# Optimization experiments

Measured on AMD Instinct MI355X. Metric: run time of the kernel, lower is better.

The kernel has to match this reference:

```python
import jax, jax.numpy as jnp
import numpy as np

act = jax.nn.softplus

def _lin(h, W, b):
    return h @ W + b

def _residual_stack(h, Ws, bs):
    # Ws: [L,2,D,D], bs: [L,2,D]; Residual: x + Lin(act(Lin(act(x))))
    for i in range(Ws.shape[0]):
        t = _lin(act(h), Ws[i, 0], bs[i, 0])
        t = _lin(act(t), Ws[i, 1], bs[i, 1])
        h = t + h
    return h

def setup_inputs() -> dict:
    key = jax.random.key(0)
    N, E, D, R = 40000, 640000, 128, 64
    n_int, n_atomic, n_out = 2, 2, 1
    ks = jax.random.split(key, 24)
    s = 1.0 / np.sqrt(D)
    sr = 1.0 / np.sqrt(R)
    inp = {
        'x': jax.random.normal(ks[0], (N, D), jnp.float32),
        'g_ij': jax.random.uniform(ks[1], (E, R), jnp.float32),
        'idx_i': jax.random.randint(ks[2], (E,), 0, N, jnp.int32),
        'idx_j': jax.random.randint(ks[3], (E,), 0, N, jnp.int32),
        'n_atoms': N,
        'u': jax.random.uniform(ks[4], (D,), jnp.float32),  # torch.rand(n_atom_basis)
        'W_g': jax.random.normal(ks[5], (R, D), jnp.float32) * sr,
        'b_g': jnp.zeros((D,), jnp.float32),
        'W_j': jax.random.normal(ks[6], (D, D), jnp.float32) * s,
        'b_j': jnp.zeros((D,), jnp.float32),
        'W_i': jax.random.normal(ks[7], (D, D), jnp.float32) * s,
        'b_i': jnp.zeros((D,), jnp.float32),
        'W_f': jax.random.normal(ks[8], (D, D), jnp.float32) * s,
        'b_f': jnp.zeros((D,), jnp.float32),
        'Wres_int': jax.random.normal(ks[9], (n_int, 2, D, D), jnp.float32) * s,
        'bres_int': jnp.zeros((n_int, 2, D), jnp.float32),
        'Wres_atom': jax.random.normal(ks[10], (n_atomic, 2, D, D), jnp.float32) * s,
        'bres_atom': jnp.zeros((n_atomic, 2, D), jnp.float32),
        'Wres_out': jax.random.normal(ks[11], (n_out, 2, D, D), jnp.float32) * s,
        'bres_out': jnp.zeros((n_out, 2, D), jnp.float32),
        'W_out': jax.random.normal(ks[12], (D, D), jnp.float32) * s,
        'b_out': jnp.zeros((D,), jnp.float32),
    }
    return inp

def reference(x, g_ij, idx_i, idx_j, n_atoms, u,
              W_g, b_g, W_j, b_j, W_i, b_i, W_f, b_f,
              Wres_int, bres_int, Wres_atom, bres_atom,
              Wres_out, bres_out, W_out, b_out):
    # --- PhysNetInteraction ---
    x_j = x[idx_j]                                   # [E,D] gather
    xp = u * x                                       # random feature scale
    vp = act(_lin(act(x_j), W_j, b_j)) * _lin(g_ij, W_g, b_g)   # [E,D]
    vm = act(_lin(act(x), W_i, b_i))                 # [N,D]
    v = jax.ops.segment_sum(vp, idx_i, num_segments=n_atoms) + vm
    v = _residual_stack(v, Wres_int, bres_int)
    v = act(v)
    h = xp + _lin(v, W_f, b_f)
    # --- atomic residuals ---
    h = _residual_stack(h, Wres_atom, bres_atom)
    # --- Output block ---
    o = _residual_stack(h, Wres_out, bres_out)
    o = _lin(act(o), W_out, b_out)
    return (o, h)
```

## Files before the change

### kernel.cpp

```cpp
#include <hip/hip_runtime.h>


#define D 128
#define TILE 64
#define LDP 136
#define SLOT 16384
#define EPB 64

typedef __attribute__((ext_vector_type(8))) short s8v;
typedef __attribute__((ext_vector_type(4))) unsigned short us4;
typedef __attribute__((ext_vector_type(4))) float f32x4;

struct Frag { f32x4 v[8]; };
struct WReg8 { s8v w[8]; };

__device__ __forceinline__ float sp_act(float x) {
    float t = __builtin_amdgcn_exp2f(-fabsf(x) * 1.44269504088896f);
    return fmaxf(x, 0.f) + 0.69314718055994f * __builtin_amdgcn_logf(1.0f + t);
}
__device__ __forceinline__ unsigned short f2bf(float f) {
    unsigned int u = __float_as_uint(f);
    u += 0x7fffu + ((u >> 16) & 1u);
    return (unsigned short)(u >> 16);
}
__device__ __forceinline__ float bf2f(unsigned short h) {
    return __uint_as_float(((unsigned int)h) << 16);
}

__global__ void prep_weights(
    const float* __restrict__ Wj, const float* __restrict__ Wi,
    const float* __restrict__ Wf, const float* __restrict__ Wout,
    const float* __restrict__ Wri, const float* __restrict__ Wra,
    const float* __restrict__ Wro, const float* __restrict__ Wg,
    unsigned short* __restrict__ wt, int* __restrict__ zbase, int zn)
{
    int id = blockIdx.x;
    if (id >= 15) {
        int i = (id - 15) * 256 + threadIdx.x;
        if (i < zn) zbase[i] = 0;
        return;
    }
    const float* src;
    int K = D;
    if      (id == 0)  src = Wj;
    else if (id == 1)  src = Wi;
    else if (id == 2)  src = Wf;
    else if (id == 3)  src = Wout;
    else if (id < 8)   src = Wri + (id - 4) * D * D;
    else if (id < 12)  src = Wra + (id - 8) * D * D;
    else if (id < 14)  src = Wro + (id - 12) * D * D;
    else             { src = Wg; K = 64; }
    unsigned short* dst = wt + id * SLOT;
    int total = K * D;
    for (int e = threadIdx.x; e < total; e += blockDim.x) {
        int k = e >> 7, n = e & 127;
        dst[n * K + k] = f2bf(src[e]);
    }
}

__device__ __forceinline__ void load_w128(const unsigned short* __restrict__ wt,
                                          unsigned short (*Wl)[LDP], int t) {
#pragma unroll
    for (int q = 0; q < 8; ++q) {
        int c = t + q * 256;
        int row = c >> 4;
        int k = (c & 15) * 8;
        *(s8v*)&Wl[row][k] = *(const s8v*)(wt + row * 128 + k);
    }
}

__device__ __forceinline__ void mm128(const unsigned short (*Ax)[LDP],
                                      const unsigned short (*Wl)[LDP],
                                      int wrow, int lane, Frag& acc) {
    int r = lane & 15, g4 = lane >> 4;
#pragma unroll
    for (int k0 = 0; k0 < 4; ++k0) {
        s8v a = *(const s8v*)&Ax[wrow + r][k0 * 32 + g4 * 8];
#pragma unroll
        for (int n = 0; n < 8; ++n) {
            s8v b = *(const s8v*)&Wl[n * 16 + r][k0 * 32 + g4 * 8];
            acc.v[n] = __builtin_amdgcn_mfma_f32_16x16x32_bf16(a, b, acc.v[n], 0, 0, 0);
        }
    }
}

__global__ __launch_bounds__(256) void node_pre(
    const float* __restrict__ x, const unsigned short* __restrict__ wt,
    const float* __restrict__ bj, const float* __restrict__ bi,
    unsigned short* __restrict__ P, float* __restrict__ v,
    const int* __restrict__ idx_i, int* __restrict__ counts, int E, int N)
{
    __shared__ __align__(16) unsigned short Ax[TILE][LDP];
    __shared__ __align__(16) unsigned short Wl[D][LDP];
    int t = threadIdx.x;
    int r0 = blockIdx.x * TILE;
#pragma unroll
    for (int q = 0; q < 8; ++q) {
        int c = t + q * 256;
        int row = c >> 5;
        int col = (c & 31) * 4;
        int gr = r0 + row;
        f32x4 xv = {0.f, 0.f, 0.f, 0.f};
        if (gr < N) xv = *(const f32x4*)(x + (size_t)gr * D + col);
        us4 w = { f2bf(sp_act(xv[0])), f2bf(sp_act(xv[1])),
                  f2bf(sp_act(xv[2])), f2bf(sp_act(xv[3])) };
        *(us4*)&Ax[row][col] = w;
    }
    load_w128(wt + 0 * SLOT, Wl, t);
    WReg8 wr;
#pragma unroll
    for (int q = 0; q < 8; ++q) {
        int c = t + q * 256; int row = c >> 4; int k = (c & 15) * 8;
        wr.w[q] = *(const s8v*)(wt + 1 * SLOT + row * 128 + k);
    }
    __syncthreads();

    int lane = t & 63, wv = t >> 6, wrow = wv * 16;
    int r = lane & 15, g4 = lane >> 4;
    Frag acc;
#pragma unroll
    for (int n = 0; n < 8; ++n) { float b = bj[n * 16 + r]; acc.v[n] = (f32x4){b, b, b, b}; }
    mm128(Ax, Wl, wrow, lane, acc);
#pragma unroll
    for (int i = 0; i < 4; ++i) {
        int row = r0 + wrow + g4 * 4 + i;
        if (row < N) {
            s8v p;
#pragma unroll
            for (int n = 0; n < 8; ++n) p[n] = (short)f2bf(sp_act(acc.v[n][i]));
            __builtin_nontemporal_store(p, (s8v*)(P + (size_t)row * D + r * 8));
        }
    }
    __syncthreads();
#pragma unroll
    for (int q = 0; q < 8; ++q) {
        int c = t + q * 256; int row = c >> 4; int k = (c & 15) * 8;
        *(s8v*)&Wl[row][k] = wr.w[q];
    }
    __syncthreads();
#pragma unroll
    for (int n = 0; n < 8; ++n) { float b = bi[n * 16 + r]; acc.v[n] = (f32x4){b, b, b, b}; }
    mm128(Ax, Wl, wrow, lane, acc);
#pragma unroll
    for (int i = 0; i < 4; ++i) {
        int row = r0 + wrow + g4 * 4 + i;
        if (row < N) {
            f32x4 lo, hi;
#pragma unroll
            for (int n = 0; n < 4; ++n) {
                lo[n] = sp_act(acc.v[n][i]);
                hi[n] = sp_act(acc.v[n + 4][i]);
            }
            __builtin_nontemporal_store(lo, (f32x4*)(v + (size_t)row * D + r * 8));
            __builtin_nontemporal_store(hi, (f32x4*)(v + (size_t)row * D + r * 8 + 4));
        }
    }
    for (int e = blockIdx.x * blockDim.x + t; e < E; e += gridDim.x * blockDim.x)
        atomicAdd(&counts[idx_i[e]], 1);
}

__global__ __launch_bounds__(1024) void scan_kernel(const int* __restrict__ counts,
                                                    int* __restrict__ offsets, int n) {
    __shared__ int wsum[16];
    int t = threadIdx.x, lane = t & 63, w = t >> 6;
    int carry = 0;
    for (int base = 0; base < n; base += 1024) {
        int i = base + t;
        int val = (i < n) ? counts[i] : 0;
        int s = val;
#pragma unroll
        for (int d = 1; d < 64; d <<= 1) {
            int y = __shfl_up(s, d, 64);
            if (lane >= d) s += y;
        }
        if (lane == 63) wsum[w] = s;
        __syncthreads();
        if (w == 0) {
            int ws = (lane < 16) ? wsum[lane] : 0;
#pragma unroll
            for (int d = 1; d < 16; d <<= 1) {
                int y = __shfl_up(ws, d, 64);
                if (lane >= d) ws += y;
            }
            if (lane < 16) wsum[lane] = ws;
        }
        __syncthreads();
        int wpre = (w == 0) ? 0 : wsum[w - 1];
        if (i < n) offsets[i] = carry + wpre + (s - val);
        int total = wsum[15];
        __syncthreads();
        carry += total;
    }
}
__global__ void scatter_kernel(const int* __restrict__ idx_i,
                               const int* __restrict__ idx_j,
                               const int* __restrict__ offsets,
                               int* __restrict__ cursor, int* __restrict__ perm,
                               int* __restrict__ sni, int* __restrict__ snj, int E) {
    for (int e = blockIdx.x * blockDim.x + threadIdx.x; e < E; e += gridDim.x * blockDim.x) {
        int i = idx_i[e];
        int p = offsets[i] + atomicAdd(&cursor[i], 1);
        perm[p] = e;
        sni[p] = i;
        snj[p] = idx_j[e];
    }
}

__global__ __launch_bounds__(256) void edge_gather(
    const float* __restrict__ g, const int* __restrict__ spe,
    const int* __restrict__ sni, const int* __restrict__ snj,
    const unsigned short* __restrict__ wtg, const float* __restrict__ bg,
    const unsigned short* __restrict__ P, float* __restrict__ v, int E)
{
    __shared__ __align__(16) unsigned char smem[27648];
    __shared__ int s_ni[EPB];
    unsigned short (*Gx)[72] = (unsigned short(*)[72])smem;
    unsigned short (*WG)[72] = (unsigned short(*)[72])(smem + 9216);
    unsigned short (*Vx)[136] = (unsigned short(*)[136])smem;

    int t = threadIdx.x;
    int e0 = blockIdx.x * EPB;
    int lane = t & 63, wv = t >> 6;
    int r = lane & 15, g4 = lane >> 4;

    if (t < EPB) {
        int e = e0 + t;
        s_ni[t] = (e < E) ? sni[e] : -1;
    }

    int pe0, pe1, pe2, pe3;
    {
        int brow = t >> 4;
        pe0 = (e0 + brow +  0 < E) ? spe[e0 + brow +  0] : -1;
        pe1 = (e0 + brow + 16 < E) ? spe[e0 + brow + 16] : -1;
        pe2 = (e0 + brow + 32 < E) ? spe[e0 + brow + 32] : -1;
        pe3 = (e0 + brow + 48 < E) ? spe[e0 + brow + 48] : -1;
    }
    {
        int col = (t & 15) * 4;
        f32x4 gv0 = {0.f,0.f,0.f,0.f}, gv1 = {0.f,0.f,0.f,0.f};
        f32x4 gv2 = {0.f,0.f,0.f,0.f}, gv3 = {0.f,0.f,0.f,0.f};
        if (pe0 >= 0) gv0 = __builtin_nontemporal_load((const f32x4*)(g + (size_t)pe0 * 64 + col));
        if (pe1 >= 0) gv1 = __builtin_nontemporal_load((const f32x4*)(g + (size_t)pe1 * 64 + col));
        if (pe2 >= 0) gv2 = __builtin_nontemporal_load((const f32x4*)(g + (size_t)pe2 * 64 + col));
        if (pe3 >= 0) gv3 = __builtin_nontemporal_load((const f32x4*)(g + (size_t)pe3 * 64 + col));
        int brow = t >> 4;
        us4 w0 = { f2bf(gv0[0]), f2bf(gv0[1]), f2bf(gv0[2]), f2bf(gv0[3]) };
        us4 w1 = { f2bf(gv1[0]), f2bf(gv1[1]), f2bf(gv1[2]), f2bf(gv1[3]) };
        us4 w2 = { f2bf(gv2[0]), f2bf(gv2[1]), f2bf(gv2[2]), f2bf(gv2[3]) };
        us4 w3 = { f2bf(gv3[0]), f2bf(gv3[1]), f2bf(gv3[2]), f2bf(gv3[3]) };
        *(us4*)&Gx[brow +  0][col] = w0;
        *(us4*)&Gx[brow + 16][col] = w1;
        *(us4*)&Gx[brow + 32][col] = w2;
        *(us4*)&Gx[brow + 48][col] = w3;
    }
#pragma unroll
    for (int q = 0; q < 4; ++q) {
        int c = t + q * 256;
        int row = c >> 3;
        int k = (c & 7) * 8;
        *(s8v*)&WG[row][k] = *(const s8v*)(wtg + row * 64 + k);
    }
    s8v pv0, pv1, pv2, pv3;
    {
        int eb = e0 + wv * 16 + g4 * 4;
        int nj0 = (eb + 0 < E) ? snj[eb + 0] : 0;
        int nj1 = (eb + 1 < E) ? snj[eb + 1] : 0;
        int nj2 = (eb + 2 < E) ? snj[eb + 2] : 0;
        int nj3 = (eb + 3 < E) ? snj[eb + 3] : 0;
        pv0 = *(const s8v*)(P + (size_t)nj0 * D + r * 8);
        pv1 = *(const s8v*)(P + (size_t)nj1 * D + r * 8);
        pv2 = *(const s8v*)(P + (size_t)nj2 * D + r * 8);
        pv3 = *(const s8v*)(P + (size_t)nj3 * D + r * 8);
    }
    __syncthreads();

    Frag acc;
#pragma unroll
    for (int n = 0; n < 8; ++n) { float b = bg[n * 16 + r]; acc.v[n] = (f32x4){b, b, b, b}; }
#pragma unroll
    for (int k0 = 0; k0 < 2; ++k0) {
        s8v a = *(const s8v*)&Gx[wv * 16 + r][k0 * 32 + g4 * 8];
#pragma unroll
        for (int n = 0; n < 8; ++n) {
            s8v b = *(const s8v*)&WG[n * 16 + r][k0 * 32 + g4 * 8];
            acc.v[n] = __builtin_amdgcn_mfma_f32_16x16x32_bf16(a, b, acc.v[n], 0, 0, 0);
        }
    }
    __syncthreads();

#pragma unroll
    for (int i = 0; i < 4; ++i) {
        int el = wv * 16 + g4 * 4 + i;
        bool valid = (e0 + el) < E;
        s8v pvv = (i == 0) ? pv0 : (i == 1) ? pv1 : (i == 2) ? pv2 : pv3;
        s8v outv;
#pragma unroll
        for (int n = 0; n < 8; ++n) {
            float val = valid ? acc.v[n][i] * bf2f((unsigned short)pvv[n]) : 0.f;
            outv[n] = (short)f2bf(val);
        }
        *(s8v*)&Vx[el][r * 8] = outv;
    }
    __syncthreads();

    int f = t & 127, half = t >> 7;
    int estart = half * 32;
    int ecap = E - e0; if (ecap > EPB) ecap = EPB;
    int eend = estart + 32; if (eend > ecap) eend = ecap;
    if (estart < eend) {
        float accv = 0.f;
        int cur = s_ni[estart];
        for (int e = estart; e < eend; ++e) {
            int node = s_ni[e];
            if (node != cur) {
                unsafeAtomicAdd(v + (size_t)cur * D + f, accv);
                accv = 0.f; cur = node;
            }
            accv += bf2f(Vx[e][f]);
        }
        unsafeAtomicAdd(v + (size_t)cur * D + f, accv);
    }
}

__device__ __forceinline__ void stage_w(WReg8& wr,
                                        const unsigned short* __restrict__ wtp, int t) {
#pragma unroll
    for (int q = 0; q < 8; ++q) {
        int c = t + q * 256; int row = c >> 4; int k = (c & 15) * 8;
        wr.w[q] = *(const s8v*)(wtp + row * 128 + k);
    }
}

template <bool RESID>
__device__ __forceinline__ Frag do_layer(
    const Frag in, const Frag resid,
    const float* __restrict__ bias,
    WReg8& wreg, const unsigned short* __restrict__ next_wt,
    unsigned short (*Ax)[LDP], unsigned short (*Wl)[LDP],
    int t, int lane, int wrow, int r, int g4)
{
    __syncthreads();
#pragma unroll
    for (int n = 0; n < 8; ++n)
#pragma unroll
        for (int i = 0; i < 4; ++i)
            Ax[wrow + g4 * 4 + i][n * 16 + r] = f2bf(sp_act(in.v[n][i]));
#pragma unroll
    for (int q = 0; q < 8; ++q) {
        int c = t + q * 256; int row = c >> 4; int k = (c & 15) * 8;
        *(s8v*)&Wl[row][k] = wreg.w[q];
    }
    if (next_wt) stage_w(wreg, next_wt, t);
    __syncthreads();
    Frag out;
#pragma unroll
    for (int n = 0; n < 8; ++n) {
        float b = bias[n * 16 + r];
        f32x4 bb = {b, b, b, b};
        out.v[n] = RESID ? bb + resid.v[n] : bb;
    }
    mm128(Ax, Wl, wrow, lane, out);
    return out;
}

__device__ __forceinline__ void store_tile(
    const Frag val, float* __restrict__ dst, int r0, int N,
    float (*St)[132], int t, int wv, int r, int g4)
{
    int wrow = wv * 16;
    __syncthreads();
#pragma unroll
    for (int n = 0; n < 8; ++n)
#pragma unroll
        for (int i = 0; i < 4; ++i)
            St[wrow + g4 * 4 + i][n * 16 + r] = val.v[n][i];
    __syncthreads();
#pragma unroll
    for (int q = 0; q < 8; ++q) {
        int idx = t + q * 256;
        int row = idx >> 5, c4 = (idx & 31) * 4;
        int gr = r0 + row;
        if (gr < N) {
            f32x4 vv = *(const f32x4*)&St[row][c4];
            __builtin_nontemporal_store(vv, (f32x4*)(dst + (size_t)gr * D + c4));
        }
    }
}

__global__ __launch_bounds__(256) void phaseB(
    const float* __restrict__ vin, const float* __restrict__ x,
    const float* __restrict__ u, const unsigned short* __restrict__ wt,
    const float* __restrict__ bri, const float* __restrict__ bra,
    const float* __restrict__ bro, const float* __restrict__ bfv,
    const float* __restrict__ bout,
    float* __restrict__ o_out, float* __restrict__ h_out, int N)
{
    __shared__ __align__(16) unsigned short Ax[TILE][LDP];
    __shared__ __align__(16) unsigned short Wl[D][LDP];
    float (*St)[132] = (float(*)[132])Wl;
    int t = threadIdx.x, lane = t & 63, wv = t >> 6, wrow = wv * 16;
    int r = lane & 15, g4 = lane >> 4;
    int r0 = blockIdx.x * TILE;

    WReg8 wreg;
    stage_w(wreg, wt + 4 * SLOT, t);

    Frag h;
#pragma unroll
    for (int i = 0; i < 4; ++i) {
        int row = r0 + wrow + g4 * 4 + i;
        f32x4 lo = {0.f, 0.f, 0.f, 0.f}, hi = {0.f, 0.f, 0.f, 0.f};
        if (row < N) {
            lo = __builtin_nontemporal_load((const f32x4*)(vin + (size_t)row * D + r * 8));
            hi = __builtin_nontemporal_load((const f32x4*)(vin + (size_t)row * D + r * 8 + 4));
        }
#pragma unroll
        for (int n = 0; n < 4; ++n) { h.v[n][i] = lo[n]; h.v[n + 4][i] = hi[n]; }
    }

    Frag t0;
    t0 = do_layer<false>(h,  h, bri + 0 * D, wreg, wt +  5 * SLOT, Ax, Wl, t, lane, wrow, r, g4);
    h  = do_layer<true >(t0, h, bri + 1 * D, wreg, wt +  6 * SLOT, Ax, Wl, t, lane, wrow, r, g4);
    t0 = do_layer<false>(h,  h, bri + 2 * D, wreg, wt +  7 * SLOT, Ax, Wl, t, lane, wrow, r, g4);
    h  = do_layer<true >(t0, h, bri + 3 * D, wreg, wt +  2 * SLOT, Ax, Wl, t, lane, wrow, r, g4);
    Frag ux;
#pragma unroll
    for (int n = 0; n < 8; ++n)
#pragma unroll
        for (int i = 0; i < 4; ++i) {
            int row = r0 + wrow + g4 * 4 + i;
            float xv = (row < N) ? x[(size_t)row * D + n * 16 + r] : 0.f;
            ux.v[n][i] = u[n * 16 + r] * xv;
        }
    h  = do_layer<true >(h,  ux, bfv, wreg, wt + 8 * SLOT, Ax, Wl, t, lane, wrow, r, g4);
    t0 = do_layer<false>(h,  h, bra + 0 * D, wreg, wt +  9 * SLOT, Ax, Wl, t, lane, wrow, r, g4);
    h  = do_layer<true >(t0, h, bra + 1 * D, wreg, wt + 10 * SLOT, Ax, Wl, t, lane, wrow, r, g4);
    t0 = do_layer<false>(h,  h, bra + 2 * D, wreg, wt + 11 * SLOT, Ax, Wl, t, lane, wrow, r, g4);
    h  = do_layer<true >(t0, h, bra + 3 * D, wreg, wt + 12 * SLOT, Ax, Wl, t, lane, wrow, r, g4);
    store_tile(h, h_out, r0, N, St, t, wv, r, g4);
    t0 = do_layer<false>(h,  h, bro + 0 * D, wreg, wt + 13 * SLOT, Ax, Wl, t, lane, wrow, r, g4);
    h  = do_layer<true >(t0, h, bro + 1 * D, wreg, wt +  3 * SLOT, Ax, Wl, t, lane, wrow, r, g4);
    t0 = do_layer<false>(h,  h, bout,        wreg, nullptr,        Ax, Wl, t, lane, wrow, r, g4);
    store_tile(t0, o_out, r0, N, St, t, wv, r, g4);
}

extern "C" void kernel_launch(void* const* d_in, const int* in_sizes, int n_in,
                              void* d_out, int out_size, void* d_ws, size_t ws_size,
                              hipStream_t stream)
{
    const float* x     = (const float*)d_in[0];
    const float* g     = (const float*)d_in[1];
    const int*   idx_i = (const int*)d_in[2];
    const int*   idx_j = (const int*)d_in[3];
    const float* u     = (const float*)d_in[5];
    const float* Wg    = (const float*)d_in[6];
    const float* bg    = (const float*)d_in[7];
    const float* Wj    = (const float*)d_in[8];
    const float* bj    = (const float*)d_in[9];
    const float* Wi    = (const float*)d_in[10];
    const float* bi    = (const float*)d_in[11];
    const float* Wf    = (const float*)d_in[12];
    const float* bf    = (const float*)d_in[13];
    const float* Wri   = (const float*)d_in[14];
    const float* bri   = (const float*)d_in[15];
    const float* Wra   = (const float*)d_in[16];
    const float* bra   = (const float*)d_in[17];
    const float* Wro   = (const float*)d_in[18];
    const float* bro   = (const float*)d_in[19];
    const float* Wout  = (const float*)d_in[20];
    const float* bout  = (const float*)d_in[21];

    int N = in_sizes[0] / D;
    int E = in_sizes[2];

    float* out = (float*)d_out;
    float* v     = out;
    float* h_out = out + (size_t)N * D;
    unsigned short* P = (unsigned short*)h_out;
    unsigned short* wt = (unsigned short*)d_ws;

    int* ibase   = (int*)(out + (size_t)N * D + (size_t)N * D / 2);
    int* counts  = ibase;
    int* offsets = ibase + N;
    int* cursor  = ibase + 2 * (size_t)N;
    int* perm    = ibase + 3 * (size_t)N;
    int* sni     = perm + E;
    int* snj     = sni + E;

    int zn = 3 * N;
    prep_weights<<<15 + (zn + 255) / 256, 256, 0, stream>>>(
        Wj, Wi, Wf, Wout, Wri, Wra, Wro, Wg, wt, ibase, zn);

    int nb = (N + TILE - 1) / TILE;
    node_pre<<<nb, 256, 0, stream>>>(x, wt, bj, bi, P, v, idx_i, counts, E, N);

    scan_kernel<<<1, 1024, 0, stream>>>(counts, offsets, N);
    scatter_kernel<<<1024, 256, 0, stream>>>(idx_i, idx_j, offsets, cursor,
                                             perm, sni, snj, E);

    int eb = (E + EPB - 1) / EPB;
    edge_gather<<<eb, 256, 0, stream>>>(g, perm, sni, snj, wt + 14 * SLOT, bg,
                                        P, v, E);

    phaseB<<<nb, 256, 0, stream>>>(v, x, u, wt, bri, bra, bro, bf, bout,
                                   out, h_out, N);
}
```

Measured before the change: 295.9 us.

## Vectorize scan, drop nontemporal hints, and shrink LDS padding in edge gather

The scan kernel now processes eight counts per thread with vector loads and a serial per-thread prefix, cutting the number of outer iterations over the 40000 nodes. The P store and the permuted g_ij loads switch from nontemporal to regular cached accesses, so P can stay in cache for the later gather. The Gx/WG LDS row padding drops from 72 to 68 elements to shrink shared memory per block. The narrower padding may bring back LDS bank conflicts in the MFMA operand reads.

```diff
diff --git a/kernel.cpp b/kernel.cpp
--- a/kernel.cpp
+++ b/kernel.cpp
@@ -6,10 +6,12 @@
 #define LDP 136
 #define SLOT 16384
 #define EPB 64
+#define WPAD 68
 
 typedef __attribute__((ext_vector_type(8))) short s8v;
 typedef __attribute__((ext_vector_type(4))) unsigned short us4;
 typedef __attribute__((ext_vector_type(4))) float f32x4;
+typedef __attribute__((ext_vector_type(4))) int i32x4;
 
 struct Frag { f32x4 v[8]; };
 struct WReg8 { s8v w[8]; };
@@ -128,7 +130,7 @@
             s8v p;
 #pragma unroll
             for (int n = 0; n < 8; ++n) p[n] = (short)f2bf(sp_act(acc.v[n][i]));
-            __builtin_nontemporal_store(p, (s8v*)(P + (size_t)row * D + r * 8));
+            *(s8v*)(P + (size_t)row * D + r * 8) = p;
         }
     }
     __syncthreads();
@@ -164,10 +166,22 @@
     __shared__ int wsum[16];
     int t = threadIdx.x, lane = t & 63, w = t >> 6;
     int carry = 0;
-    for (int base = 0; base < n; base += 1024) {
-        int i = base + t;
-        int val = (i < n) ? counts[i] : 0;
-        int s = val;
+    for (int base = 0; base < n; base += 8192) {
+        int i0 = base + t * 8;
+        int vals[8];
+        if (i0 + 7 < n) {
+            i32x4 a = *(const i32x4*)(counts + i0);
+            i32x4 b = *(const i32x4*)(counts + i0 + 4);
+#pragma unroll
+            for (int k = 0; k < 4; ++k) { vals[k] = a[k]; vals[k + 4] = b[k]; }
+        } else {
+#pragma unroll
+            for (int k = 0; k < 8; ++k) vals[k] = (i0 + k < n) ? counts[i0 + k] : 0;
+        }
+        int tsum = 0;
+#pragma unroll
+        for (int k = 0; k < 8; ++k) tsum += vals[k];
+        int s = tsum;
 #pragma unroll
         for (int d = 1; d < 64; d <<= 1) {
             int y = __shfl_up(s, d, 64);
@@ -186,7 +200,13 @@
         }
         __syncthreads();
         int wpre = (w == 0) ? 0 : wsum[w - 1];
-        if (i < n) offsets[i] = carry + wpre + (s - val);
+        int run = carry + wpre + (s - tsum);
+#pragma unroll
+        for (int k = 0; k < 8; ++k) {
+            int i = i0 + k;
+            if (i < n) offsets[i] = run;
+            run += vals[k];
+        }
         int total = wsum[15];
         __syncthreads();
         carry += total;
@@ -212,10 +232,10 @@
     const unsigned short* __restrict__ wtg, const float* __restrict__ bg,
     const unsigned short* __restrict__ P, float* __restrict__ v, int E)
 {
-    __shared__ __align__(16) unsigned char smem[27648];
+    __shared__ __align__(16) unsigned char smem[26112];
     __shared__ int s_ni[EPB];
-    unsigned short (*Gx)[72] = (unsigned short(*)[72])smem;
-    unsigned short (*WG)[72] = (unsigned short(*)[72])(smem + 9216);
+    unsigned short (*Gx)[WPAD] = (unsigned short(*)[WPAD])smem;
+    unsigned short (*WG)[WPAD] = (unsigned short(*)[WPAD])(smem + 8704);
     unsigned short (*Vx)[136] = (unsigned short(*)[136])smem;
 
     int t = threadIdx.x;
@@ -240,10 +260,10 @@
         int col = (t & 15) * 4;
         f32x4 gv0 = {0.f,0.f,0.f,0.f}, gv1 = {0.f,0.f,0.f,0.f};
         f32x4 gv2 = {0.f,0.f,0.f,0.f}, gv3 = {0.f,0.f,0.f,0.f};
-        if (pe0 >= 0) gv0 = __builtin_nontemporal_load((const f32x4*)(g + (size_t)pe0 * 64 + col));
-        if (pe1 >= 0) gv1 = __builtin_nontemporal_load((const f32x4*)(g + (size_t)pe1 * 64 + col));
-        if (pe2 >= 0) gv2 = __builtin_nontemporal_load((const f32x4*)(g + (size_t)pe2 * 64 + col));
-        if (pe3 >= 0) gv3 = __builtin_nontemporal_load((const f32x4*)(g + (size_t)pe3 * 64 + col));
+        if (pe0 >= 0) gv0 = *(const f32x4*)(g + (size_t)pe0 * 64 + col);
+        if (pe1 >= 0) gv1 = *(const f32x4*)(g + (size_t)pe1 * 64 + col);
+        if (pe2 >= 0) gv2 = *(const f32x4*)(g + (size_t)pe2 * 64 + col);
+        if (pe3 >= 0) gv3 = *(const f32x4*)(g + (size_t)pe3 * 64 + col);
         int brow = t >> 4;
         us4 w0 = { f2bf(gv0[0]), f2bf(gv0[1]), f2bf(gv0[2]), f2bf(gv0[3]) };
         us4 w1 = { f2bf(gv1[0]), f2bf(gv1[1]), f2bf(gv1[2]), f2bf(gv1[3]) };
```

Result: slower. 332.9 us (+12.5%).
